# Performance work log

Measured on AMD Instinct MI355X. Metric: run time of the kernel, lower is better.

Reference implementation:

```python
import jax, jax.numpy as jnp
import numpy as np

VOC, EMB, C, H, W, ANS = 10000, 300, 24, 8, 8, 1000
HID = 500          # lstm_hidden_size
GH = 100           # g_mlp hidden
B, L = 64, 32
O = H * W          # obj_num
CONCAT = 2 * C + HID  # 548


def setup_inputs() -> dict:
    key = jax.random.key(0)
    ks = jax.random.split(key, 20)
    inp = {}
    inp["sent_batch"] = jax.random.randint(ks[0], (B, L), 0, VOC)
    inp["conv_map_batch"] = jax.random.normal(ks[1], (B, C, H, W), jnp.float32)
    inp["sents_lengths"] = jax.random.randint(ks[2], (B,), 1, L + 1)
    # embedding table with padding_idx=0 zeroed
    emb = jax.random.normal(ks[3], (VOC, EMB), jnp.float32) * 0.02
    inp["embed_table"] = emb.at[0].set(0.0)
    # forward-direction LSTM params (torch gate order i,f,g,o)
    s_ih = 1.0 / np.sqrt(HID)
    inp["W_ih"] = jax.random.uniform(ks[4], (4 * HID, EMB), jnp.float32, -s_ih, s_ih)
    inp["W_hh"] = jax.random.uniform(ks[5], (4 * HID, HID), jnp.float32, -s_ih, s_ih)
    inp["b_ih"] = jax.random.uniform(ks[6], (4 * HID,), jnp.float32, -s_ih, s_ih)
    inp["b_hh"] = jax.random.uniform(ks[7], (4 * HID,), jnp.float32, -s_ih, s_ih)
    # random (non-learned) LSTM initial state, as torch.rand in init_hidden
    inp["h0"] = jax.random.uniform(ks[8], (B, HID), jnp.float32)
    inp["c0"] = jax.random.uniform(ks[9], (B, HID), jnp.float32)
    def lin(k, o, i):
        s = 1.0 / np.sqrt(i)
        kw, kb = jax.random.split(k)
        return (jax.random.uniform(kw, (o, i), jnp.float32, -s, s),
                jax.random.uniform(kb, (o,), jnp.float32, -s, s))
    inp["g1_w"], inp["g1_b"] = lin(ks[10], GH, CONCAT)
    inp["g2_w"], inp["g2_b"] = lin(ks[11], GH, GH)
    inp["f1_w"], inp["f1_b"] = lin(ks[12], GH, GH)
    inp["f2_w"], inp["f2_b"] = lin(ks[13], ANS, GH)
    return inp


def _lstm_final_h(emb, lengths, W_ih, W_hh, b_ih, b_hh, h0, c0):
    # emb: (B, L, EMB); returns final forward hidden at t = length-1 per example
    xs = jnp.swapaxes(emb, 0, 1)  # (L, B, EMB)
    ts = jnp.arange(emb.shape[1])
    bias = b_ih + b_hh
    def step(carry, inp):
        h, c = carry
        xt, t = inp
        gates = xt @ W_ih.T + h @ W_hh.T + bias
        i, f, g, o = jnp.split(gates, 4, axis=-1)
        i, f, o = jax.nn.sigmoid(i), jax.nn.sigmoid(f), jax.nn.sigmoid(o)
        g = jnp.tanh(g)
        c_new = f * c + i * g
        h_new = o * jnp.tanh(c_new)
        m = (t < lengths)[:, None]
        return (jnp.where(m, h_new, h), jnp.where(m, c_new, c)), None
    (h_T, _), _ = jax.lax.scan(step, (h0, c0), (xs, ts))
    return h_T  # (B, HID)


def reference(sent_batch, conv_map_batch, sents_lengths, embed_table,
              W_ih, W_hh, b_ih, b_hh, h0, c0,
              g1_w, g1_b, g2_w, g2_b, f1_w, f1_b, f2_w, f2_b):
    emb = embed_table[sent_batch]  # (B, L, EMB)
    q = _lstm_final_h(emb, sents_lengths, W_ih, W_hh, b_ih, b_hh, h0, c0)  # (B, HID)
    obj = jnp.transpose(conv_map_batch, (0, 2, 3, 1)).reshape(B, O, C)  # (B, O, C)
    # g_mlp layer 1, split to avoid materializing (B, O^2, 548):
    # pair (i,j): cat(q, obj_j, obj_i) -> partial sums broadcast-added
    q_part = q @ g1_w[:, :HID].T                    # (B, GH)
    j_part = obj @ g1_w[:, HID:HID + C].T           # (B, O, GH) -- conv_expand_1 block
    i_part = obj @ g1_w[:, HID + C:].T              # (B, O, GH) -- conv_expand_2 block
    h1 = jax.nn.relu(q_part[:, None, None, :] + i_part[:, :, None, :]
                     + j_part[:, None, :, :] + g1_b)  # (B, O, O, GH)
    h2 = jax.nn.relu(h1 @ g2_w.T + g2_b)              # (B, O, O, GH)
    g_sum = h2.sum(axis=(1, 2))                       # (B, GH)
    f = jax.nn.relu(g_sum @ f1_w.T + f1_b)
    f = jax.nn.relu(f @ f2_w.T + f2_b)                # (B, ANS)
    return jax.nn.log_softmax(f, axis=-1)
```

## Files before the change

### kernel.cpp

```cpp
#include <hip/hip_runtime.h>
#include <cmath>

#define BATCH 64
#define SEQL  32
#define EMBD  300
#define HIDD  500
#define NOBJ  64
#define GHID  100
#define ANSN  1000
#define MCOL  2048

#define GRP    4
#define GBATCH 16
#define BPG    25
#define UPB8   20
#define NBLK   (GRP*BPG)
#define NXG    256
#define SLOTP  32

#define KPADX  328
#define TCH    4

typedef _Float16 half8 __attribute__((ext_vector_type(8)));
typedef float    f32x4 __attribute__((ext_vector_type(4)));

__device__ __forceinline__ float sigmf(float x){ return 1.f/(1.f+expf(-x)); }

__device__ __forceinline__ unsigned long long ld_cc8(const unsigned long long* p){
    return __hip_atomic_load(p, __ATOMIC_RELAXED, __HIP_MEMORY_SCOPE_AGENT);
}
__device__ __forceinline__ void st_cc8(_Float16* p, unsigned long long v){
    __hip_atomic_store((unsigned long long*)p, v, __ATOMIC_RELAXED, __HIP_MEMORY_SCOPE_AGENT);
}
__device__ __forceinline__ float ld_cc4(const float* p){
    return __hip_atomic_load(p, __ATOMIC_RELAXED, __HIP_MEMORY_SCOPE_AGENT);
}
__device__ __forceinline__ void st_cc4(float* p, float v){
    __hip_atomic_store(p, v, __ATOMIC_RELAXED, __HIP_MEMORY_SCOPE_AGENT);
}

__device__ __forceinline__ void gbarA(int* slots, int grp, int ub, int seq)
{
    __syncthreads();
    if (threadIdx.x == 0)
        __hip_atomic_store(slots + (grp*BPG + ub)*SLOTP, seq,
                           __ATOMIC_RELAXED, __HIP_MEMORY_SCOPE_AGENT);
    if (threadIdx.x < BPG){
        int* s = slots + (grp*BPG + threadIdx.x)*SLOTP;
        while (__hip_atomic_load(s, __ATOMIC_RELAXED, __HIP_MEMORY_SCOPE_AGENT) < seq)
            __builtin_amdgcn_s_sleep(1);
    }
    asm volatile("" ::: "memory");
    __syncthreads();
}

__global__ __launch_bounds__(320, 1) void k_mega(
    const int* __restrict__ sent, const float* __restrict__ table,
    const float* __restrict__ Wih, const float* __restrict__ b_ih, const float* __restrict__ b_hh,
    _Float16* __restrict__ hF, float* __restrict__ hqB, float* __restrict__ xgT,
    const float* __restrict__ Whh, const float* __restrict__ h0, const float* __restrict__ c0,
    const int* __restrict__ lens, int* __restrict__ slots, int* __restrict__ xgdone)
{
    __shared__ __align__(16) char smem[103040];

    int tid = threadIdx.x, bid = blockIdx.x;
    int w = tid >> 6, lane = tid & 63;

    if (bid >= NBLK){
        _Float16* Sh  = (_Float16*)smem;
        int*      sidx= (int*)(smem + 41984);
        int xb = bid - NBLK;
        int tc = xb >> 5;
        int n0 = (xb & 31) * 64;
        int rA = lane & 15, kb = lane >> 4;

        for (int i = tid; i < TCH*64; i += 320){
            int tt = i >> 6, b = i & 63;
            sidx[tt*64 + b] = sent[b*SEQL + tc*TCH + tt];
        }
        for (int i = tid; i < 64*75; i += 320){
            int n = i / 75, c4 = i - (i/75)*75;
            float4 v = {0.f,0.f,0.f,0.f};
            if (n0 + n < 2000)
                v = *(const float4*)(Wih + (size_t)(n0+n)*300 + c4*4);
            _Float16* dst = &Sh[n*KPADX + c4*4];
            dst[0]=(_Float16)v.x; dst[1]=(_Float16)v.y; dst[2]=(_Float16)v.z; dst[3]=(_Float16)v.w;
        }
        for (int i = tid; i < 64*20; i += 320){
            int n = i / 20, k = 300 + (i - (i/20)*20);
            Sh[n*KPADX + k] = (_Float16)0.f;
        }
        __syncthreads();
        half8 areg[10];
        float biasr[4];
        if (w < 4){
            #pragma unroll
            for (int ks = 0; ks < 10; ++ks)
                areg[ks] = *(const half8*)&Sh[(w*16 + rA)*KPADX + ks*32 + kb*8];
            #pragma unroll
            for (int r = 0; r < 4; ++r){
                int n = n0 + w*16 + kb*4 + r;
                biasr[r] = (n < 2000) ? b_ih[n] + b_hh[n] : 0.f;
            }
        }
        __syncthreads();

        for (int tt = 0; tt < TCH; ++tt){
            for (int i = tid; i < 64*75; i += 320){
                int m = i / 75, c4 = i - (i/75)*75;
                float4 v = *(const float4*)(table + (size_t)sidx[tt*64 + m]*300 + c4*4);
                _Float16* dst = &Sh[m*KPADX + c4*4];
                dst[0]=(_Float16)v.x; dst[1]=(_Float16)v.y; dst[2]=(_Float16)v.z; dst[3]=(_Float16)v.w;
            }
            for (int i = tid; i < 64*20; i += 320){
                int m = i / 20, k = 300 + (i - (i/20)*20);
                Sh[m*KPADX + k] = (_Float16)0.f;
            }
            __syncthreads();

            if (w < 4){
                f32x4 acc[4] = {};
                #pragma unroll
                for (int ks = 0; ks < 10; ++ks){
                    #pragma unroll
                    for (int mc = 0; mc < 4; ++mc){
                        half8 bf = *(const half8*)&Sh[(mc*16 + rA)*KPADX + ks*32 + kb*8];
                        acc[mc] = __builtin_amdgcn_mfma_f32_16x16x32_f16(areg[ks], bf, acc[mc], 0, 0, 0);
                    }
                }
                #pragma unroll
                for (int r = 0; r < 4; ++r){
                    int n = n0 + w*16 + kb*4 + r;
                    if (n < 2000){
                        #pragma unroll
                        for (int mc = 0; mc < 4; ++mc)
                            st_cc4(xgT + (size_t)n*MCOL + (tc*TCH+tt)*64 + mc*16 + rA,
                                   acc[mc][r] + biasr[r]);
                    }
                }
            }
            __syncthreads();
        }
        if (tid == 0)
            __hip_atomic_fetch_add(xgdone + tc*SLOTP, 1,
                                   __ATOMIC_RELAXED, __HIP_MEMORY_SCOPE_AGENT);
        return;
    }

    _Float16* Wl  = (_Float16*)smem;
    float*    gl  = (float*)(smem + 81920);
    _Float16* hout= (_Float16*)(smem + 102400);

    int grp = bid / BPG, ub = bid - grp*BPG;
    int u0  = ub * UPB8;

    int pb  = tid & 15, puu = tid >> 4;
    int pu  = u0 + puu;
    int gb  = grp*GBATCH + pb;
    float cprev = c0[gb*HIDD + pu];
    float hprev = h0[gb*HIDD + pu];
    int   mylen = lens[gb];
    hout[pb*UPB8 + puu] = (_Float16)hprev;

    for (int i = tid; i < 80*512; i += 320){
        int m = i >> 9, k = i & 511;
        int g = m / UPB8, uu = m - g*UPB8;
        float v = (k < HIDD) ? Whh[(size_t)(g*HIDD + u0 + uu)*HIDD + k] : 0.f;
        int off = (i*2) ^ ((m & 7) << 4);
        *(_Float16*)((char*)Wl + off) = (_Float16)v;
    }
    __syncthreads();
    if (tid < 80){
        int b = tid / 5, q = tid - (tid/5)*5;
        unsigned long long v = *(const unsigned long long*)((const char*)hout + b*40 + q*8);
        st_cc8(hF + ((size_t)(1*GRP + grp)*GBATCH + b)*512 + u0 + q*4, v);
    }
    if (ub == 0 && tid >= 128 && tid < 224){
        int j = tid - 128;
        int buf = j / 48, r = j - buf*48;
        int b = r / 3, q = r - (r/3)*3;
        st_cc8(hF + ((size_t)(buf*GRP + grp)*GBATCH + b)*512 + 500 + q*4, 0ULL);
    }
    gbarA(slots, grp, ub, 1);

    const int mA = lane & 15, kb = lane >> 4;

    for (int t = 0; t < SEQL; ++t){
        if ((t & 3) == 0){
            if (tid == 0){
                const int* f = xgdone + (t >> 2)*SLOTP;
                while (__hip_atomic_load(f, __ATOMIC_RELAXED, __HIP_MEMORY_SCOPE_AGENT) < 32)
                    __builtin_amdgcn_s_sleep(1);
            }
            asm volatile("" ::: "memory");
            __syncthreads();
        }

        const _Float16* hsrc = hF + (size_t)(((t&1)^1)*GRP + grp)*GBATCH*512;

        float xgv[4];
        #pragma unroll
        for (int g = 0; g < 4; ++g)
            xgv[g] = ld_cc4(xgT + (size_t)(g*HIDD + pu)*MCOL + t*64 + gb);

        if (w < 4){
            half8 bf[4];
            #pragma unroll
            for (int ks4 = 0; ks4 < 4; ++ks4){
                int ke = (w*4 + ks4)*32 + kb*8;
                const unsigned long long* p =
                    (const unsigned long long*)(hsrc + mA*512 + ke);
                union { unsigned long long q[2]; half8 h; } u;
                u.q[0] = ld_cc8(p);
                u.q[1] = ld_cc8(p + 1);
                bf[ks4] = u.h;
            }
            f32x4 acc[5] = {};
            #pragma unroll
            for (int rt = 0; rt < 5; ++rt){
                #pragma unroll
                for (int ks4 = 0; ks4 < 4; ++ks4){
                    int kByte = (w*4 + ks4)*64 + kb*16;
                    int m = rt*16 + mA;
                    int aOff = (m*1024 + kByte) ^ ((m & 7) << 4);
                    half8 af = *(const half8*)((const char*)Wl + aOff);
                    acc[rt] = __builtin_amdgcn_mfma_f32_16x16x32_f16(af, bf[ks4], acc[rt], 0, 0, 0);
                }
            }
            #pragma unroll
            for (int rt = 0; rt < 5; ++rt)
                #pragma unroll
                for (int r = 0; r < 4; ++r)
                    gl[(w*80 + rt*16 + kb*4 + r)*16 + mA] = acc[rt][r];
        }
        __syncthreads();

        {
            float g4[4];
            #pragma unroll
            for (int g = 0; g < 4; ++g){
                int row = g*UPB8 + puu;
                float s = gl[(0*80 + row)*16 + pb] + gl[(1*80 + row)*16 + pb]
                        + gl[(2*80 + row)*16 + pb] + gl[(3*80 + row)*16 + pb];
                s += xgv[g];
                g4[g] = s;
            }
            float si = sigmf(g4[0]), sf = sigmf(g4[1]);
            float tg = tanhf(g4[2]), so = sigmf(g4[3]);
            float cn = sf*cprev + si*tg;
            float hn = so*tanhf(cn);
            if (t < mylen){ cprev = cn; hprev = hn; }
            hout[pb*UPB8 + puu] = (_Float16)hprev;
            if (t == SEQL-1) hqB[(size_t)gb*512 + pu] = hprev;
        }
        if (t < SEQL-1){
            __syncthreads();
            if (tid < 80){
                int b = tid / 5, q = tid - (tid/5)*5;
                unsigned long long v = *(const unsigned long long*)((const char*)hout + b*40 + q*8);
                st_cc8(hF + ((size_t)((t&1)*GRP + grp)*GBATCH + b)*512 + u0 + q*4, v);
            }
            gbarA(slots, grp, ub, t + 2);
        }
    }
}

__global__ __launch_bounds__(256, 1) void k_pair2(
    const float* __restrict__ hqB, const float* __restrict__ conv,
    const float* __restrict__ g1w, const float* __restrict__ g1b,
    const float* __restrict__ g2w, const float* __restrict__ g2b,
    float* __restrict__ part)
{
    __shared__ float    convl[24][64];
    __shared__ float    g1ij[100][48];
    __shared__ float    hb[512];
    __shared__ float    qpl[112];
    __shared__ float    jpl[NOBJ][132];
    __shared__ float    basel[16][132];
    __shared__ _Float16 g2h[112][136];
    __shared__ float    redx[4][112];

    int b  = blockIdx.x >> 2;
    int ic = blockIdx.x & 3;
    int tid = threadIdx.x;
    int w = tid >> 6, lane = tid & 63;
    int ncol = lane & 15, kb = lane >> 4;

    for (int i = tid; i < 24*64; i += 256)
        convl[i>>6][i&63] = conv[((size_t)b*24 + (i>>6))*64 + (i&63)];
    for (int i = tid; i < 100*48; i += 256){
        int n = i/48, c = i - (i/48)*48;
        g1ij[n][c] = g1w[(size_t)n*548 + 500 + c];
    }
    for (int i = tid; i < 512; i += 256) hb[i] = hqB[(size_t)b*512 + i];
    for (int i = tid; i < 112*136; i += 256){
        int n = i/136, k = i - (i/136)*136;
        g2h[n][k] = (n < 100 && k < 100) ? (_Float16)g2w[n*GHID + k] : (_Float16)0.f;
    }
    __syncthreads();

    if (tid < 100){
        const float4* wr = (const float4*)(g1w + (size_t)tid*548);
        float s = g1b[tid];
        #pragma unroll 5
        for (int k4 = 0; k4 < 125; ++k4){
            float4 v = wr[k4];
            s += v.x*hb[k4*4] + v.y*hb[k4*4+1] + v.z*hb[k4*4+2] + v.w*hb[k4*4+3];
        }
        qpl[tid] = s;
    }
    for (int i = tid; i < NOBJ*100; i += 256){
        int o = i / 100, n = i - (i/100)*100;
        float sj = 0.f;
        #pragma unroll
        for (int c = 0; c < 24; ++c) sj += convl[c][o] * g1ij[n][c];
        jpl[o][n] = sj;
    }
    for (int i = tid; i < NOBJ*32; i += 256) jpl[i>>5][100 + (i&31)] = 0.f;
    __syncthreads();

    for (int i = tid; i < 16*132; i += 256){
        int il = i / 132, k = i - (i/132)*132;
        float v = 0.f;
        if (k < 100){
            float si = 0.f;
            int o = ic*16 + il;
            #pragma unroll
            for (int c = 0; c < 24; ++c) si += convl[c][o] * g1ij[k][24+c];
            v = qpl[k] + si;
        }
        basel[il][k] = v;
    }
    float gb7[7];
    #pragma unroll
    for (int nt = 0; nt < 7; ++nt){
        int n = nt*16 + ncol;
        gb7[nt] = (n < 100) ? g2b[n] : 0.f;
    }
    __syncthreads();

    f32x4 sacc[7] = {};
    #pragma unroll
    for (int it = 0; it < 4; ++it){
        int il = w*4 + it;
        #pragma unroll
        for (int jc = 0; jc < 4; ++jc){
            f32x4 acc[7] = {};
            int jrow = jc*16 + ncol;
            #pragma unroll
            for (int ks = 0; ks < 4; ++ks){
                int k0 = ks*32 + kb*8;
                const float* jpp = &jpl[jrow][k0];
                const float* bpp = &basel[il][k0];
                half8 af;
                #pragma unroll
                for (int e = 0; e < 8; ++e)
                    af[e] = (_Float16)fmaxf(jpp[e] + bpp[e], 0.f);
                #pragma unroll
                for (int nt = 0; nt < 7; ++nt){
                    half8 bf = *(const half8*)&g2h[nt*16 + ncol][k0];
                    acc[nt] = __builtin_amdgcn_mfma_f32_16x16x32_f16(af, bf, acc[nt], 0, 0, 0);
                }
            }
            #pragma unroll
            for (int nt = 0; nt < 7; ++nt)
                #pragma unroll
                for (int r = 0; r < 4; ++r)
                    sacc[nt][r] += fmaxf(acc[nt][r] + gb7[nt], 0.f);
        }
    }
    #pragma unroll
    for (int nt = 0; nt < 7; ++nt){
        float s = sacc[nt][0] + sacc[nt][1] + sacc[nt][2] + sacc[nt][3];
        s += __shfl_xor(s, 16);
        s += __shfl_xor(s, 32);
        if (lane < 16) redx[w][nt*16 + lane] = s;
    }
    __syncthreads();
    if (tid < 100){
        float p = redx[0][tid] + redx[1][tid] + redx[2][tid] + redx[3][tid];
        part[(size_t)(b*4 + ic)*GHID + tid] = p;
    }
}

__global__ __launch_bounds__(256) void k_final(const float* __restrict__ part, const float* __restrict__ f1w,
               const float* __restrict__ f1b, const float* __restrict__ f2w,
               const float* __restrict__ f2b, float* __restrict__ out)
{
    int b = blockIdx.x;
    int tid = threadIdx.x;
    __shared__ float gs[GHID];
    __shared__ float fh[GHID];
    __shared__ float lg[ANSN];
    __shared__ float red[4], red2[4];
    if (tid < GHID){
        float s = 0.f;
        for (int ic = 0; ic < 4; ++ic) s += part[((size_t)b*4 + ic)*GHID + tid];
        gs[tid] = s;
    }
    __syncthreads();
    if (tid < GHID){
        float s = f1b[tid];
        const float* w = f1w + tid*GHID;
        for (int k = 0; k < GHID; ++k) s += gs[k]*w[k];
        fh[tid] = fmaxf(s, 0.f);
    }
    __syncthreads();
    for (int n = tid; n < ANSN; n += 256){
        float s = f2b[n];
        const float* w = f2w + (size_t)n*GHID;
        for (int k = 0; k < GHID; ++k) s += fh[k]*w[k];
        lg[n] = fmaxf(s, 0.f);
    }
    __syncthreads();
    float mx = -1e30f;
    for (int n = tid; n < ANSN; n += 256) mx = fmaxf(mx, lg[n]);
    #pragma unroll
    for (int off = 32; off > 0; off >>= 1) mx = fmaxf(mx, __shfl_xor(mx, off));
    if ((tid & 63) == 0) red[tid >> 6] = mx;
    __syncthreads();
    mx = fmaxf(fmaxf(red[0], red[1]), fmaxf(red[2], red[3]));
    float se = 0.f;
    for (int n = tid; n < ANSN; n += 256) se += expf(lg[n]-mx);
    #pragma unroll
    for (int off = 32; off > 0; off >>= 1) se += __shfl_xor(se, off);
    if ((tid & 63) == 0) red2[tid >> 6] = se;
    __syncthreads();
    se = red2[0]+red2[1]+red2[2]+red2[3];
    float lse = logf(se);
    for (int n = tid; n < ANSN; n += 256) out[(size_t)b*ANSN + n] = lg[n] - mx - lse;
}

extern "C" void kernel_launch(void* const* d_in, const int* in_sizes, int n_in,
                              void* d_out, int out_size, void* d_ws, size_t ws_size,
                              hipStream_t stream)
{
    const int*   sent  = (const int*)  d_in[0];
    const float* conv  = (const float*)d_in[1];
    const int*   lens  = (const int*)  d_in[2];
    const float* table = (const float*)d_in[3];
    const float* W_ih  = (const float*)d_in[4];
    const float* W_hh  = (const float*)d_in[5];
    const float* b_ih  = (const float*)d_in[6];
    const float* b_hh  = (const float*)d_in[7];
    const float* h0    = (const float*)d_in[8];
    const float* c0    = (const float*)d_in[9];
    const float* g1_w  = (const float*)d_in[10];
    const float* g1_b  = (const float*)d_in[11];
    const float* g2_w  = (const float*)d_in[12];
    const float* g2_b  = (const float*)d_in[13];
    const float* f1_w  = (const float*)d_in[14];
    const float* f1_b  = (const float*)d_in[15];
    const float* f2_w  = (const float*)d_in[16];
    const float* f2_b  = (const float*)d_in[17];
    float* out = (float*)d_out;

    float* ws    = (float*)d_ws;
    int*   slots = (int*)d_ws;
    int*   xgdone= (int*)d_ws + NBLK*SLOTP;
    _Float16* hF = (_Float16*)(ws + 16384);
    float* hqB  = ws + 16384 + 32768;
    float* xgT  = hqB + 64*512;
    float* part = xgT + (size_t)4*HIDD*MCOL;

    hipMemsetAsync(slots, 0, 16384, stream);

    k_mega<<<NBLK + NXG, 320, 0, stream>>>(sent, table, W_ih, b_ih, b_hh,
                                           hF, hqB, xgT, W_hh, h0, c0, lens,
                                           slots, xgdone);

    k_pair2<<<BATCH*4, 256, 0, stream>>>(hqB, conv, g1_w, g1_b, g2_w, g2_b, part);

    k_final<<<BATCH, 256, 0, stream>>>(part, f1_w, f1_b, f2_w, f2_b, out);
}
```

Before: 226.6 us.

## Fuse final MLP into pair kernel via last-block counter; shuffle-pack LSTM hidden stores

Folds the k_final head (f1, f2, log_softmax) into the pair kernel. The last of the four blocks per batch element, found with an atomic counter, runs the head, which removes one kernel launch and the gap before it. Inside the LSTM step, the hidden state is now packed to fp16 with wave shuffles and written straight to global memory. This drops the shared-memory staging buffer and one __syncthreads per timestep on the serial recurrence. The head loops also switch to float4 weight loads, and the memset is resized to cover the new counters.

Result: no change. 223.9 us (-1.2%).

```diff
diff --git a/kernel.cpp b/kernel.cpp
--- a/kernel.cpp
+++ b/kernel.cpp
@@ -54,6 +54,26 @@
     __syncthreads();
 }
 
+__device__ __forceinline__ void pack_store_h(
+    _Float16* hF, int buf, int grp, int u0, int w, int lane, float hval)
+{
+    union { _Float16 f; unsigned short s; } cv;
+    cv.f = (_Float16)hval;
+    unsigned int h2 = cv.s;
+    int base = lane & 15;
+    unsigned int x0 = (unsigned int)__shfl((int)h2, base +  0, 64);
+    unsigned int x1 = (unsigned int)__shfl((int)h2, base + 16, 64);
+    unsigned int x2 = (unsigned int)__shfl((int)h2, base + 32, 64);
+    unsigned int x3 = (unsigned int)__shfl((int)h2, base + 48, 64);
+    if (lane < 16){
+        unsigned long long v = (unsigned long long)(x0 & 0xFFFFu)
+                             | ((unsigned long long)(x1 & 0xFFFFu) << 16)
+                             | ((unsigned long long)(x2 & 0xFFFFu) << 32)
+                             | ((unsigned long long)(x3 & 0xFFFFu) << 48);
+        st_cc8(hF + ((size_t)(buf*GRP + grp)*GBATCH + lane)*512 + u0 + w*4, v);
+    }
+}
+
 __global__ __launch_bounds__(320, 1) void k_mega(
     const int* __restrict__ sent, const float* __restrict__ table,
     const float* __restrict__ Wih, const float* __restrict__ b_ih, const float* __restrict__ b_hh,
@@ -61,7 +81,7 @@
     const float* __restrict__ Whh, const float* __restrict__ h0, const float* __restrict__ c0,
     const int* __restrict__ lens, int* __restrict__ slots, int* __restrict__ xgdone)
 {
-    __shared__ __align__(16) char smem[103040];
+    __shared__ __align__(16) char smem[102400];
 
     int tid = threadIdx.x, bid = blockIdx.x;
     int w = tid >> 6, lane = tid & 63;
@@ -149,7 +169,6 @@
 
     _Float16* Wl  = (_Float16*)smem;
     float*    gl  = (float*)(smem + 81920);
-    _Float16* hout= (_Float16*)(smem + 102400);
 
     int grp = bid / BPG, ub = bid - grp*BPG;
     int u0  = ub * UPB8;
@@ -160,7 +179,6 @@
     float cprev = c0[gb*HIDD + pu];
     float hprev = h0[gb*HIDD + pu];
     int   mylen = lens[gb];
-    hout[pb*UPB8 + puu] = (_Float16)hprev;
 
     for (int i = tid; i < 80*512; i += 320){
         int m = i >> 9, k = i & 511;
@@ -169,12 +187,7 @@
         int off = (i*2) ^ ((m & 7) << 4);
         *(_Float16*)((char*)Wl + off) = (_Float16)v;
     }
-    __syncthreads();
-    if (tid < 80){
-        int b = tid / 5, q = tid - (tid/5)*5;
-        unsigned long long v = *(const unsigned long long*)((const char*)hout + b*40 + q*8);
-        st_cc8(hF + ((size_t)(1*GRP + grp)*GBATCH + b)*512 + u0 + q*4, v);
-    }
+    pack_store_h(hF, 1, grp, u0, w, lane, hprev);
     if (ub == 0 && tid >= 128 && tid < 224){
         int j = tid - 128;
         int buf = j / 48, r = j - buf*48;
@@ -250,26 +263,23 @@
             float cn = sf*cprev + si*tg;
             float hn = so*tanhf(cn);
             if (t < mylen){ cprev = cn; hprev = hn; }
-            hout[pb*UPB8 + puu] = (_Float16)hprev;
-            if (t == SEQL-1) hqB[(size_t)gb*512 + pu] = hprev;
-        }
-        if (t < SEQL-1){
-            __syncthreads();
-            if (tid < 80){
-                int b = tid / 5, q = tid - (tid/5)*5;
-                unsigned long long v = *(const unsigned long long*)((const char*)hout + b*40 + q*8);
-                st_cc8(hF + ((size_t)((t&1)*GRP + grp)*GBATCH + b)*512 + u0 + q*4, v);
-            }
+        }
+        if (t == SEQL-1){
+            hqB[(size_t)gb*512 + pu] = hprev;
+        } else {
+            pack_store_h(hF, t & 1, grp, u0, w, lane, hprev);
             gbarA(slots, grp, ub, t + 2);
         }
     }
 }
 
-__global__ __launch_bounds__(256, 1) void k_pair2(
+__global__ __launch_bounds__(256, 1) void k_pair3(
     const float* __restrict__ hqB, const float* __restrict__ conv,
     const float* __restrict__ g1w, const float* __restrict__ g1b,
     const float* __restrict__ g2w, const float* __restrict__ g2b,
-    float* __restrict__ part)
+    const float* __restrict__ f1w, const float* __restrict__ f1b,
+    const float* __restrict__ f2w, const float* __restrict__ f2b,
+    float* __restrict__ part, int* __restrict__ pcnt, float* __restrict__ out)
 {
     __shared__ float    convl[24][64];
     __shared__ float    g1ij[100][48];
@@ -279,6 +289,10 @@
     __shared__ float    basel[16][132];
     __shared__ _Float16 g2h[112][136];
     __shared__ float    redx[4][112];
+    __shared__ float    gs[112], fh[112];
+    __shared__ float    lg[ANSN];
+    __shared__ float    red[4], red2[4];
+    __shared__ int      lastf;
 
     int b  = blockIdx.x >> 2;
     int ic = blockIdx.x & 3;
@@ -379,37 +393,45 @@
     __syncthreads();
     if (tid < 100){
         float p = redx[0][tid] + redx[1][tid] + redx[2][tid] + redx[3][tid];
-        part[(size_t)(b*4 + ic)*GHID + tid] = p;
-    }
-}
-
-__global__ __launch_bounds__(256) void k_final(const float* __restrict__ part, const float* __restrict__ f1w,
-               const float* __restrict__ f1b, const float* __restrict__ f2w,
-               const float* __restrict__ f2b, float* __restrict__ out)
-{
-    int b = blockIdx.x;
-    int tid = threadIdx.x;
-    __shared__ float gs[GHID];
-    __shared__ float fh[GHID];
-    __shared__ float lg[ANSN];
-    __shared__ float red[4], red2[4];
-    if (tid < GHID){
+        st_cc4(part + (size_t)(b*4 + ic)*GHID + tid, p);
+    }
+    __syncthreads();
+
+    if (tid == 0){
+        int old = __hip_atomic_fetch_add(pcnt + b*SLOTP, 1,
+                                         __ATOMIC_ACQ_REL, __HIP_MEMORY_SCOPE_AGENT);
+        lastf = (old == 3);
+    }
+    __syncthreads();
+    if (!lastf) return;
+
+    if (tid < 100){
         float s = 0.f;
-        for (int ic = 0; ic < 4; ++ic) s += part[((size_t)b*4 + ic)*GHID + tid];
+        #pragma unroll
+        for (int ic2 = 0; ic2 < 4; ++ic2)
+            s += ld_cc4(part + (size_t)(b*4 + ic2)*GHID + tid);
         gs[tid] = s;
     }
     __syncthreads();
-    if (tid < GHID){
+    if (tid < 100){
+        const float4* wr = (const float4*)(f1w + (size_t)tid*GHID);
         float s = f1b[tid];
-        const float* w = f1w + tid*GHID;
-        for (int k = 0; k < GHID; ++k) s += gs[k]*w[k];
+        #pragma unroll 5
+        for (int k4 = 0; k4 < 25; ++k4){
+            float4 v = wr[k4];
+            s += v.x*gs[k4*4] + v.y*gs[k4*4+1] + v.z*gs[k4*4+2] + v.w*gs[k4*4+3];
+        }
         fh[tid] = fmaxf(s, 0.f);
     }
     __syncthreads();
     for (int n = tid; n < ANSN; n += 256){
+        const float4* wr = (const float4*)(f2w + (size_t)n*GHID);
         float s = f2b[n];
-        const float* w = f2w + (size_t)n*GHID;
-        for (int k = 0; k < GHID; ++k) s += fh[k]*w[k];
+        #pragma unroll 5
+        for (int k4 = 0; k4 < 25; ++k4){
+            float4 v = wr[k4];
+            s += v.x*fh[k4*4] + v.y*fh[k4*4+1] + v.z*fh[k4*4+2] + v.w*fh[k4*4+3];
+        }
         lg[n] = fmaxf(s, 0.f);
     }
     __syncthreads();
@@ -458,18 +480,18 @@
     float* ws    = (float*)d_ws;
     int*   slots = (int*)d_ws;
     int*   xgdone= (int*)d_ws + NBLK*SLOTP;
+    int*   pcnt  = (int*)d_ws + NBLK*SLOTP + 8*SLOTP;
     _Float16* hF = (_Float16*)(ws + 16384);
     float* hqB  = ws + 16384 + 32768;
     float* xgT  = hqB + 64*512;
     float* part = xgT + (size_t)4*HIDD*MCOL;
 
-    hipMemsetAsync(slots, 0, 16384, stream);
+    hipMemsetAsync(slots, 0, (NBLK + 8 + BATCH)*SLOTP*sizeof(int), stream);
 
     k_mega<<<NBLK + NXG, 320, 0, stream>>>(sent, table, W_ih, b_ih, b_hh,
                                            hF, hqB, xgT, W_hh, h0, c0, lens,
                                            slots, xgdone);
 
-    k_pair2<<<BATCH*4, 256, 0, stream>>>(hqB, conv, g1_w, g1_b, g2_w, g2_b, part);
-
-    k_final<<<BATCH, 256, 0, stream>>>(part, f1_w, f1_b, f2_w, f2_b, out);
-}
+    k_pair3<<<BATCH*4, 256, 0, stream>>>(hqB, conv, g1_w, g1_b, g2_w, g2_b,
+                                         f1_w, f1_b, f2_w, f2_b, part, pcnt, out);
+}
```
